# Kernel optimization log

Measured on AMD Instinct MI355X. Metric: run time of the kernel, lower is better.

Reference implementation:

```python
import jax, jax.numpy as jnp
import numpy as np
from jax import lax

B, H, W, CIN = 64, 32, 32, 64
COUT = 64
KH, KW = 3, 3
STRIDES = (1, 1)
H_OUT, W_OUT = H // STRIDES[0], W // STRIDES[1]
KFEAT = KH * KW * CIN  # flattened receptive-field size per location


def setup_inputs() -> dict:
    key = jax.random.key(0)
    k_in, k_ker, k_b = jax.random.split(key, 3)
    inputs = jax.random.normal(k_in, (B, H, W, CIN), dtype=jnp.float32)
    # lecun_normal over fan_in = KFEAT for the unshared local kernel
    kernel = jax.random.normal(k_ker, (H_OUT, W_OUT, KFEAT, COUT), dtype=jnp.float32) / np.sqrt(KFEAT).astype(np.float32)
    bias = jnp.zeros((H_OUT, W_OUT, COUT), dtype=jnp.float32)
    return {"inputs": inputs, "kernel": kernel, "bias": bias}


def reference(inputs, kernel, bias) -> jnp.ndarray:
    # Locally-connected conv: per-spatial-location unshared weights.
    # XLA lowers this to patch extraction + batched per-location matmuls.
    y = lax.conv_general_dilated_local(
        inputs, kernel, STRIDES, 'SAME',
        filter_shape=(KH, KW),
        dimension_numbers=('NHWC', 'HWIO', 'NHWC'))  # [B, H_OUT, W_OUT, COUT]
    y = y + bias[None]
    return y
```

## Files before the change

kernel.cpp:

```cpp
#include <hip/hip_runtime.h>
#include <hip/hip_bf16.h>

#define BATCH 64
#define HH 32
#define WW 32
#define CIN 64
#define COUT 64
#define KFEAT 576

typedef __bf16 bf16x8 __attribute__((ext_vector_type(8)));
typedef float f32x4 __attribute__((ext_vector_type(4)));

static __device__ __forceinline__ ushort f2bf_bits(float f) {
  __bf16 b = (__bf16)f;
  return __builtin_bit_cast(ushort, b);
}

__global__ __launch_bounds__(256, 4) void LocalConv_kernel(
    const float* __restrict__ in, const float* __restrict__ ker,
    const float* __restrict__ bias, float* __restrict__ out) {
  __shared__ __align__(16) ushort Ab[2][64 * 64];

  const int orig = blockIdx.x;
  const int hw = (orig & 7) * 128 + (orig >> 3);
  const int h = hw >> 5, w = hw & 31;
  const int hm = h % 3, wm = w % 3;
  const int tid = threadIdx.x;
  const int lane = tid & 63;
  const int wave = tid >> 6;

  const float* kerhw = ker + (size_t)hw * (KFEAT * COUT);

  auto offs = [&](int t, int& hp, int& wp, int& p) {
    const int t3 = t / 3, t0 = t % 3;
    const int dh = ((t3 + 4 - hm) % 3) - 1;
    const int dw = ((t0 + 4 - wm) % 3) - 1;
    hp = h + dh;
    wp = w + dw;
    p = (dh + 1) * 3 + (dw + 1);
  };

  float4 st[4];

  auto issue = [&](int hp, int wp) {
    const bool ok = ((unsigned)hp < (unsigned)HH) && ((unsigned)wp < (unsigned)WW);
    const float* src = in + ((size_t)hp * WW + wp) * CIN;
#pragma unroll
    for (int i = 0; i < 4; ++i) {
      const int c = i * 256 + tid;
      const int brow = c >> 4;
      const int c16 = c & 15;
      if (ok) {
        st[i] = *reinterpret_cast<const float4*>(
            src + (size_t)brow * (HH * WW * CIN) + c16 * 4);
      } else {
        st[i] = make_float4(0.f, 0.f, 0.f, 0.f);
      }
    }
  };

  auto writebuf = [&](int buf_idx) {
    ushort* buf = &Ab[buf_idx][0];
#pragma unroll
    for (int i = 0; i < 4; ++i) {
      const int c = i * 256 + tid;
      const int brow = c >> 4, c16 = c & 15;
      union { ushort us[4]; uint2 u2; } pk;
      pk.us[0] = f2bf_bits(st[i].x);
      pk.us[1] = f2bf_bits(st[i].y);
      pk.us[2] = f2bf_bits(st[i].z);
      pk.us[3] = f2bf_bits(st[i].w);
      const int byteofs = brow * 128 + ((c16 * 8) ^ ((brow & 7) << 4));
      *reinterpret_cast<uint2*>(reinterpret_cast<char*>(buf) + byteofs) = pk.u2;
    }
  };

  f32x4 acc[4];
#pragma unroll
  for (int m = 0; m < 4; ++m) acc[m] = (f32x4){0.f, 0.f, 0.f, 0.f};

  const int co = wave * 16 + (lane & 15);
  const int kgrp = lane >> 4;

  int hp, wp, p;
  offs(0, hp, wp, p);
  issue(hp, wp);
  writebuf(0);
  __syncthreads();

  for (int t = 0; t < 9; ++t) {
    int pcur = p;
    if (t < 8) {
      offs(t + 1, hp, wp, p);
      issue(hp, wp);
    }

    const ushort* buf = &Ab[t & 1][0];
    const float* kp = kerhw + pcur * COUT + co;
#pragma unroll
    for (int ks = 0; ks < 2; ++ks) {
      const int ci0 = ks * 32 + kgrp * 8;
      bf16x8 bfrag;
#pragma unroll
      for (int j = 0; j < 8; ++j)
        bfrag[j] = (__bf16)kp[(size_t)(ci0 + j) * KFEAT];
#pragma unroll
      for (int m = 0; m < 4; ++m) {
        const int row = m * 16 + (lane & 15);
        const int byteofs =
            row * 128 + ((ks * 64 + kgrp * 16) ^ ((row & 7) << 4));
        bf16x8 afrag = *reinterpret_cast<const bf16x8*>(
            reinterpret_cast<const char*>(buf) + byteofs);
        acc[m] = __builtin_amdgcn_mfma_f32_16x16x32_bf16(afrag, bfrag, acc[m],
                                                         0, 0, 0);
      }
    }

    __syncthreads();
    if (t < 8) {
      writebuf((t + 1) & 1);
      __syncthreads();
    }
  }

  const float bv = bias[hw * COUT + co];
#pragma unroll
  for (int m = 0; m < 4; ++m) {
#pragma unroll
    for (int r = 0; r < 4; ++r) {
      const int b = m * 16 + kgrp * 4 + r;
      out[((size_t)b * (HH * WW) + hw) * COUT + co] = acc[m][r] + bv;
    }
  }
}

extern "C" void kernel_launch(void* const* d_in, const int* in_sizes, int n_in,
                              void* d_out, int out_size, void* d_ws,
                              size_t ws_size, hipStream_t stream) {
  const float* in = (const float*)d_in[0];
  const float* ker = (const float*)d_in[1];
  const float* bias = (const float*)d_in[2];
  float* out = (float*)d_out;
  (void)in_sizes; (void)n_in; (void)out_size; (void)d_ws; (void)ws_size;
  LocalConv_kernel<<<dim3(HH * WW), dim3(256), 0, stream>>>(in, ker, bias, out);
}
```

Baseline: 35.26 us.

## Split reduction across waves with 32x32 MFMA and LDS-reduced vectorized epilogue

Changes the work split from each wave owning 16 output channels to each wave owning a 16-channel slice of the input-channel reduction over the full 64x64 tile. It uses 32x32x16 bf16 MFMAs, and the four waves' partial sums are reduced serially through shared memory. The epilogue then writes float4 outputs with bias. This gives contiguous 32-wide weight loads and coalesced vector stores, at the cost of four serialized LDS reduction passes with extra barriers and larger accumulator register use.

```diff
diff --git a/kernel.cpp b/kernel.cpp
--- a/kernel.cpp
+++ b/kernel.cpp
@@ -9,7 +9,7 @@
 #define KFEAT 576
 
 typedef __bf16 bf16x8 __attribute__((ext_vector_type(8)));
-typedef float f32x4 __attribute__((ext_vector_type(4)));
+typedef float f32x16 __attribute__((ext_vector_type(16)));
 
 static __device__ __forceinline__ ushort f2bf_bits(float f) {
   __bf16 b = (__bf16)f;
@@ -42,7 +42,9 @@
 
   float4 st[4];
 
-  auto issue = [&](int hp, int wp) {
+  auto issue_step = [&](int t) {
+    int hp, wp, pu;
+    offs(t, hp, wp, pu);
     const bool ok = ((unsigned)hp < (unsigned)HH) && ((unsigned)wp < (unsigned)WW);
     const float* src = in + ((size_t)hp * WW + wp) * CIN;
 #pragma unroll
@@ -75,45 +77,51 @@
     }
   };
 
-  f32x4 acc[4];
+  const int l31 = lane & 31;
+  const int khalf = lane >> 5;
+  const int ci_lo = wave * 16 + khalf * 8;
+
+  f32x16 acc[2][2];
 #pragma unroll
-  for (int m = 0; m < 4; ++m) acc[m] = (f32x4){0.f, 0.f, 0.f, 0.f};
+  for (int mt = 0; mt < 2; ++mt)
+#pragma unroll
+    for (int nt = 0; nt < 2; ++nt)
+#pragma unroll
+      for (int r = 0; r < 16; ++r) acc[mt][nt][r] = 0.f;
 
-  const int co = wave * 16 + (lane & 15);
-  const int kgrp = lane >> 4;
-
-  int hp, wp, p;
-  offs(0, hp, wp, p);
-  issue(hp, wp);
+  issue_step(0);
   writebuf(0);
   __syncthreads();
 
   for (int t = 0; t < 9; ++t) {
-    int pcur = p;
-    if (t < 8) {
-      offs(t + 1, hp, wp, p);
-      issue(hp, wp);
+    if (t < 8) issue_step(t + 1);
+
+    int hh_, ww_, pcur;
+    offs(t, hh_, ww_, pcur);
+
+    const float* kpw = kerhw + pcur * COUT + l31 + (size_t)ci_lo * KFEAT;
+
+    bf16x8 bf[2];
+#pragma unroll
+    for (int nt = 0; nt < 2; ++nt) {
+      float wf[8];
+#pragma unroll
+      for (int j = 0; j < 8; ++j) wf[j] = kpw[(size_t)j * KFEAT + nt * 32];
+#pragma unroll
+      for (int j = 0; j < 8; ++j) bf[nt][j] = (__bf16)wf[j];
     }
 
     const ushort* buf = &Ab[t & 1][0];
-    const float* kp = kerhw + pcur * COUT + co;
 #pragma unroll
-    for (int ks = 0; ks < 2; ++ks) {
-      const int ci0 = ks * 32 + kgrp * 8;
-      bf16x8 bfrag;
+    for (int mt = 0; mt < 2; ++mt) {
+      const int row = mt * 32 + l31;
+      const int byteofs = row * 128 + ((ci_lo * 2) ^ ((row & 7) << 4));
+      bf16x8 af = *reinterpret_cast<const bf16x8*>(
+          reinterpret_cast<const char*>(buf) + byteofs);
 #pragma unroll
-      for (int j = 0; j < 8; ++j)
-        bfrag[j] = (__bf16)kp[(size_t)(ci0 + j) * KFEAT];
-#pragma unroll
-      for (int m = 0; m < 4; ++m) {
-        const int row = m * 16 + (lane & 15);
-        const int byteofs =
-            row * 128 + ((ks * 64 + kgrp * 16) ^ ((row & 7) << 4));
-        bf16x8 afrag = *reinterpret_cast<const bf16x8*>(
-            reinterpret_cast<const char*>(buf) + byteofs);
-        acc[m] = __builtin_amdgcn_mfma_f32_16x16x32_bf16(afrag, bfrag, acc[m],
-                                                         0, 0, 0);
-      }
+      for (int nt = 0; nt < 2; ++nt)
+        acc[mt][nt] = __builtin_amdgcn_mfma_f32_32x32x16_bf16(
+            af, bf[nt], acc[mt][nt], 0, 0, 0);
     }
 
     __syncthreads();
@@ -123,14 +131,37 @@
     }
   }
 
-  const float bv = bias[hw * COUT + co];
+  float* Cbuf = reinterpret_cast<float*>(&Ab[0][0]);
+  __syncthreads();
+#pragma unroll 1
+  for (int r = 0; r < 4; ++r) {
+    if (wave == r) {
 #pragma unroll
-  for (int m = 0; m < 4; ++m) {
+      for (int mt = 0; mt < 2; ++mt)
 #pragma unroll
-    for (int r = 0; r < 4; ++r) {
-      const int b = m * 16 + kgrp * 4 + r;
-      out[((size_t)b * (HH * WW) + hw) * COUT + co] = acc[m][r] + bv;
+        for (int nt = 0; nt < 2; ++nt)
+#pragma unroll
+          for (int g = 0; g < 16; ++g) {
+            const int row = mt * 32 + (g & 3) + 8 * (g >> 2) + 4 * khalf;
+            const int col = nt * 32 + l31;
+            if (r == 0)
+              Cbuf[row * 64 + col] = acc[mt][nt][g];
+            else
+              Cbuf[row * 64 + col] += acc[mt][nt][g];
+          }
     }
+    __syncthreads();
+  }
+
+  const int co4 = (tid & 15) * 4;
+  const float4 bv4 = *reinterpret_cast<const float4*>(bias + hw * COUT + co4);
+#pragma unroll
+  for (int i = 0; i < 4; ++i) {
+    const int b = (tid >> 4) + i * 16;
+    float4 v = *reinterpret_cast<const float4*>(&Cbuf[b * 64 + co4]);
+    v.x += bv4.x; v.y += bv4.y; v.z += bv4.z; v.w += bv4.w;
+    *reinterpret_cast<float4*>(
+        out + ((size_t)b * (HH * WW) + hw) * COUT + co4) = v;
   }
 }
 
```

Result: slower. 48.22 us (+36.8%).

## Stage kernel weights through LDS and coalesce output stores via shared memory

Applied to the files above, without the earlier changes.

Weight tiles, previously read as scalar strided global loads per lane, are now fetched as coalesced float4 loads into registers. They are converted to bf16 and written into a double-buffered swizzled LDS tile, pipelined alongside the input tile. The epilogue also moves accumulators through LDS so output rows can be written as contiguous float4 stores. This adds 16KB of LDS and extra barriers, which may reduce occupancy.

```diff
diff --git a/kernel.cpp b/kernel.cpp
--- a/kernel.cpp
+++ b/kernel.cpp
@@ -1,7 +1,6 @@
 #include <hip/hip_runtime.h>
 #include <hip/hip_bf16.h>
 
-#define BATCH 64
 #define HH 32
 #define WW 32
 #define CIN 64
@@ -20,6 +19,7 @@
     const float* __restrict__ in, const float* __restrict__ ker,
     const float* __restrict__ bias, float* __restrict__ out) {
   __shared__ __align__(16) ushort Ab[2][64 * 64];
+  __shared__ __align__(16) ushort Bb[2][64 * 64];
 
   const int orig = blockIdx.x;
   const int hw = (orig & 7) * 128 + (orig >> 3);
@@ -40,37 +40,67 @@
     p = (dh + 1) * 3 + (dw + 1);
   };
 
-  float4 st[4];
+  float4 stA[4], stB[4];
 
-  auto issue = [&](int hp, int wp) {
+  auto issueA = [&](int t) {
+    int hp, wp, pu;
+    offs(t, hp, wp, pu);
     const bool ok = ((unsigned)hp < (unsigned)HH) && ((unsigned)wp < (unsigned)WW);
     const float* src = in + ((size_t)hp * WW + wp) * CIN;
 #pragma unroll
     for (int i = 0; i < 4; ++i) {
       const int c = i * 256 + tid;
-      const int brow = c >> 4;
-      const int c16 = c & 15;
+      const int brow = c >> 4, c16 = c & 15;
       if (ok) {
-        st[i] = *reinterpret_cast<const float4*>(
+        stA[i] = *reinterpret_cast<const float4*>(
             src + (size_t)brow * (HH * WW * CIN) + c16 * 4);
       } else {
-        st[i] = make_float4(0.f, 0.f, 0.f, 0.f);
+        stA[i] = make_float4(0.f, 0.f, 0.f, 0.f);
       }
     }
   };
 
-  auto writebuf = [&](int buf_idx) {
-    ushort* buf = &Ab[buf_idx][0];
+  auto issueB = [&](int t) {
+    int hp, wp, p;
+    offs(t, hp, wp, p);
+    const float* src = kerhw + p * COUT;
+#pragma unroll
+    for (int i = 0; i < 4; ++i) {
+      const int c = i * 256 + tid;
+      const int ci = c >> 4, co4 = c & 15;
+      stB[i] = *reinterpret_cast<const float4*>(
+          src + (size_t)ci * KFEAT + co4 * 4);
+    }
+  };
+
+  auto writeA = [&](int bi) {
+    ushort* buf = &Ab[bi][0];
 #pragma unroll
     for (int i = 0; i < 4; ++i) {
       const int c = i * 256 + tid;
       const int brow = c >> 4, c16 = c & 15;
       union { ushort us[4]; uint2 u2; } pk;
-      pk.us[0] = f2bf_bits(st[i].x);
-      pk.us[1] = f2bf_bits(st[i].y);
-      pk.us[2] = f2bf_bits(st[i].z);
-      pk.us[3] = f2bf_bits(st[i].w);
+      pk.us[0] = f2bf_bits(stA[i].x);
+      pk.us[1] = f2bf_bits(stA[i].y);
+      pk.us[2] = f2bf_bits(stA[i].z);
+      pk.us[3] = f2bf_bits(stA[i].w);
       const int byteofs = brow * 128 + ((c16 * 8) ^ ((brow & 7) << 4));
+      *reinterpret_cast<uint2*>(reinterpret_cast<char*>(buf) + byteofs) = pk.u2;
+    }
+  };
+
+  auto writeB = [&](int bi) {
+    ushort* buf = &Bb[bi][0];
+#pragma unroll
+    for (int i = 0; i < 4; ++i) {
+      const int c = i * 256 + tid;
+      const int ci = c >> 4, co4 = c & 15;
+      union { ushort us[4]; uint2 u2; } pk;
+      pk.us[0] = f2bf_bits(stB[i].x);
+      pk.us[1] = f2bf_bits(stB[i].y);
+      pk.us[2] = f2bf_bits(stB[i].z);
+      pk.us[3] = f2bf_bits(stB[i].w);
+      const int byteofs = ci * 128 + ((co4 * 8) ^ (((ci >> 3) & 3) << 5));
       *reinterpret_cast<uint2*>(reinterpret_cast<char*>(buf) + byteofs) = pk.u2;
     }
   };
@@ -82,35 +112,37 @@
   const int co = wave * 16 + (lane & 15);
   const int kgrp = lane >> 4;
 
-  int hp, wp, p;
-  offs(0, hp, wp, p);
-  issue(hp, wp);
-  writebuf(0);
+  issueA(0);
+  issueB(0);
+  writeA(0);
+  writeB(0);
   __syncthreads();
 
   for (int t = 0; t < 9; ++t) {
-    int pcur = p;
     if (t < 8) {
-      offs(t + 1, hp, wp, p);
-      issue(hp, wp);
+      issueA(t + 1);
+      issueB(t + 1);
     }
 
-    const ushort* buf = &Ab[t & 1][0];
-    const float* kp = kerhw + pcur * COUT + co;
+    const ushort* bufA = &Ab[t & 1][0];
+    const ushort* bufB = &Bb[t & 1][0];
 #pragma unroll
     for (int ks = 0; ks < 2; ++ks) {
-      const int ci0 = ks * 32 + kgrp * 8;
       bf16x8 bfrag;
 #pragma unroll
-      for (int j = 0; j < 8; ++j)
-        bfrag[j] = (__bf16)kp[(size_t)(ci0 + j) * KFEAT];
+      for (int j = 0; j < 8; ++j) {
+        const int ci = ks * 32 + kgrp * 8 + j;
+        const int byteofs = ci * 128 + ((co * 2) ^ (((ci >> 3) & 3) << 5));
+        bfrag[j] = __builtin_bit_cast(__bf16, *reinterpret_cast<const ushort*>(
+            reinterpret_cast<const char*>(bufB) + byteofs));
+      }
 #pragma unroll
       for (int m = 0; m < 4; ++m) {
         const int row = m * 16 + (lane & 15);
         const int byteofs =
             row * 128 + ((ks * 64 + kgrp * 16) ^ ((row & 7) << 4));
         bf16x8 afrag = *reinterpret_cast<const bf16x8*>(
-            reinterpret_cast<const char*>(buf) + byteofs);
+            reinterpret_cast<const char*>(bufA) + byteofs);
         acc[m] = __builtin_amdgcn_mfma_f32_16x16x32_bf16(afrag, bfrag, acc[m],
                                                          0, 0, 0);
       }
@@ -118,19 +150,32 @@
 
     __syncthreads();
     if (t < 8) {
-      writebuf((t + 1) & 1);
+      writeA((t + 1) & 1);
+      writeB((t + 1) & 1);
       __syncthreads();
     }
   }
 
+  float* C = reinterpret_cast<float*>(&Ab[0][0]);
   const float bv = bias[hw * COUT + co];
 #pragma unroll
   for (int m = 0; m < 4; ++m) {
 #pragma unroll
     for (int r = 0; r < 4; ++r) {
       const int b = m * 16 + kgrp * 4 + r;
-      out[((size_t)b * (HH * WW) + hw) * COUT + co] = acc[m][r] + bv;
+      C[b * 64 + (co ^ (((b >> 2) & 3) << 4))] = acc[m][r] + bv;
     }
+  }
+  __syncthreads();
+
+  const int co4q = (tid & 15) * 4;
+#pragma unroll
+  for (int i = 0; i < 4; ++i) {
+    const int b = (tid >> 4) + i * 16;
+    const float4 v = *reinterpret_cast<const float4*>(
+        &C[b * 64 + (co4q ^ (((b >> 2) & 3) << 4))]);
+    *reinterpret_cast<float4*>(
+        out + ((size_t)b * (HH * WW) + hw) * COUT + co4q) = v;
   }
 }
 
```

New measurement: 34.85 us. Within noise of the previous version (-1.2%).
